# Optimization experiments

Hardware: AMD Instinct MI355X
Metric: run time of the kernel (lower is better)

Reference implementation:

```python
import jax, jax.numpy as jnp
import numpy as np

NEG_INF = -1e9


def setup_inputs() -> dict:
    key = jax.random.key(0)
    k1, k2, k3, k4 = jax.random.split(key, 4)
    B, H, M, N, D = 8, 16, 1024, 1024, 64
    return {
        "query": jax.random.normal(k1, (B, H, M, D), dtype=jnp.float32),
        "key": jax.random.normal(k2, (B, H, N, D), dtype=jnp.float32),
        "value": jax.random.normal(k3, (B, H, N, D), dtype=jnp.float32),
        "mask": jax.random.randint(k4, (B, H, N), 0, 2, dtype=jnp.int32),
    }


def reference(query, key, value, mask):
    # NOTE: faithful to source bug: scale uses key.size(-1) AFTER transpose,
    # i.e. N (sequence length), not d_h.
    N = key.shape[-2]
    scale = 1.0 / jnp.sqrt(jnp.asarray(N, dtype=query.dtype))
    # scores: [B, H, M, N]
    scores = jnp.einsum("bhmd,bhnd->bhmn", query, key) * scale
    scores = jnp.where(mask[:, :, None, :] == 0, jnp.asarray(NEG_INF, scores.dtype), scores)
    p_attn = jax.nn.softmax(scores, axis=-1)
    out = jnp.einsum("bhmn,bhnd->bhmd", p_attn, value)
    return out, p_attn
```

## Files before the change

kernel.cpp:

```cpp
#include <hip/hip_runtime.h>
#include <hip/hip_bf16.h>

#define BH 128
#define SEQ 1024
#define DH 64
#define MT 16
#define NW 256
#define PSTRIDE 1032

typedef __attribute__((ext_vector_type(8))) short short8;
typedef __attribute__((ext_vector_type(4))) float float4v;

__device__ __forceinline__ short bf16_rne(float x) {
    unsigned u = __builtin_bit_cast(unsigned, x);
    unsigned r = (u + 0x7fffu + ((u >> 16) & 1u)) >> 16;
    return (short)r;
}

__device__ __forceinline__ void bf16_split(float x, short& hi, short& lo) {
    unsigned u = __builtin_bit_cast(unsigned, x);
    hi = (short)(u >> 16);
    float hf = __builtin_bit_cast(float, u & 0xffff0000u);
    float res = x - hf;
    unsigned v = __builtin_bit_cast(unsigned, res);
    lo = (short)((v + 0x7fffu + ((v >> 16) & 1u)) >> 16);
}

__global__ __launch_bounds__(256, 2)
void Attention_66889820668421_kernel(const float* __restrict__ Q,
                                     const float* __restrict__ K,
                                     const float* __restrict__ V,
                                     const int*   __restrict__ mask,
                                     float* __restrict__ out,
                                     float* __restrict__ pattn)
{
    __shared__ short P_lds[MT * PSTRIDE];
    __shared__ float out_red[4][MT][DH];
    __shared__ float red_max[4][MT];
    __shared__ float red_sum[4][MT];

    const int tid  = threadIdx.x;
    const int wave = tid >> 6;
    const int lane = tid & 63;
    const int q    = lane >> 4;
    const int l    = lane & 15;
    const int bh   = blockIdx.y;
    const int m0   = blockIdx.x * MT;
    const int nbase = wave * NW;

    short8 a_hi[2], a_lo[2];
    {
        const float* qrow = Q + (size_t)(bh * SEQ + m0 + l) * DH;
        #pragma unroll
        for (int s = 0; s < 2; ++s) {
            float4v x0 = *(const float4v*)(qrow + s * 32 + q * 8);
            float4v x1 = *(const float4v*)(qrow + s * 32 + q * 8 + 4);
            #pragma unroll
            for (int j = 0; j < 4; ++j) {
                short h, lo2;
                bf16_split(x0[j], h, lo2); a_hi[s][j] = h; a_lo[s][j] = lo2;
                bf16_split(x1[j], h, lo2); a_hi[s][4 + j] = h; a_lo[s][4 + j] = lo2;
            }
        }
    }

    float4v acc[16];
    int mv[16];
    #pragma unroll
    for (int t = 0; t < 16; ++t) {
        const int key = nbase + t * 16 + l;
        const float* krow = K + (size_t)(bh * SEQ + key) * DH;
        float4v a = {0.f, 0.f, 0.f, 0.f};
        #pragma unroll
        for (int s = 0; s < 2; ++s) {
            float4v x0 = *(const float4v*)(krow + s * 32 + q * 8);
            float4v x1 = *(const float4v*)(krow + s * 32 + q * 8 + 4);
            short8 bhh, bll;
            #pragma unroll
            for (int j = 0; j < 4; ++j) {
                short h, lo2;
                bf16_split(x0[j], h, lo2); bhh[j] = h; bll[j] = lo2;
                bf16_split(x1[j], h, lo2); bhh[4 + j] = h; bll[4 + j] = lo2;
            }
            a = __builtin_amdgcn_mfma_f32_16x16x32_bf16(a_hi[s], bhh, a, 0, 0, 0);
            a = __builtin_amdgcn_mfma_f32_16x16x32_bf16(a_hi[s], bll, a, 0, 0, 0);
            a = __builtin_amdgcn_mfma_f32_16x16x32_bf16(a_lo[s], bhh, a, 0, 0, 0);
        }
        mv[t] = mask[bh * SEQ + nbase + t * 16 + l];
        acc[t] = a;
    }

    const float scale = 0.03125f;
    float pm[4] = {-3e38f, -3e38f, -3e38f, -3e38f};
    #pragma unroll
    for (int t = 0; t < 16; ++t) {
        const bool ok = (mv[t] != 0);
        #pragma unroll
        for (int r = 0; r < 4; ++r) {
            float s = ok ? acc[t][r] * scale : -1e9f;
            acc[t][r] = s;
            pm[r] = fmaxf(pm[r], s);
        }
    }
    #pragma unroll
    for (int off = 1; off < 16; off <<= 1) {
        #pragma unroll
        for (int r = 0; r < 4; ++r)
            pm[r] = fmaxf(pm[r], __shfl_xor(pm[r], off));
    }
    if (l == 0) {
        #pragma unroll
        for (int r = 0; r < 4; ++r) red_max[wave][q * 4 + r] = pm[r];
    }
    __syncthreads();

    float rm[4];
    #pragma unroll
    for (int r = 0; r < 4; ++r) {
        const int row = q * 4 + r;
        rm[r] = fmaxf(fmaxf(red_max[0][row], red_max[1][row]),
                      fmaxf(red_max[2][row], red_max[3][row]));
    }

    float ps[4] = {0.f, 0.f, 0.f, 0.f};
    #pragma unroll
    for (int t = 0; t < 16; ++t) {
        #pragma unroll
        for (int r = 0; r < 4; ++r) {
            float e = __expf(acc[t][r] - rm[r]);
            acc[t][r] = e;
            ps[r] += e;
        }
    }
    #pragma unroll
    for (int off = 1; off < 16; off <<= 1) {
        #pragma unroll
        for (int r = 0; r < 4; ++r)
            ps[r] += __shfl_xor(ps[r], off);
    }
    if (l == 0) {
        #pragma unroll
        for (int r = 0; r < 4; ++r) red_sum[wave][q * 4 + r] = ps[r];
    }
    __syncthreads();

    float inv[4];
    #pragma unroll
    for (int r = 0; r < 4; ++r) {
        const int row = q * 4 + r;
        inv[r] = 1.0f / (red_sum[0][row] + red_sum[1][row] +
                         red_sum[2][row] + red_sum[3][row]);
    }

    float* prow = pattn + ((size_t)bh * SEQ + m0) * SEQ;
    #pragma unroll
    for (int t = 0; t < 16; ++t) {
        const int col = nbase + t * 16 + l;
        #pragma unroll
        for (int r = 0; r < 4; ++r) {
            const int row = q * 4 + r;
            float p = acc[t][r] * inv[r];
            prow[(size_t)row * SEQ + col] = p;
            P_lds[row * PSTRIDE + col] = bf16_rne(p);
        }
    }
    __syncthreads();

    float4v ao[4];
    #pragma unroll
    for (int dt = 0; dt < 4; ++dt) ao[dt] = (float4v){0.f, 0.f, 0.f, 0.f};

    #pragma unroll 2
    for (int step = 0; step < 8; ++step) {
        const int key0 = nbase + step * 32;
        short8 pa = *(const short8*)&P_lds[l * PSTRIDE + key0 + q * 8];
        const float* vbase = V + (size_t)(bh * SEQ + key0 + q * 8) * DH + l;
        #pragma unroll
        for (int dt = 0; dt < 4; ++dt) {
            short8 vb;
            #pragma unroll
            for (int j = 0; j < 8; ++j)
                vb[j] = bf16_rne(vbase[(size_t)j * DH + dt * 16]);
            ao[dt] = __builtin_amdgcn_mfma_f32_16x16x32_bf16(pa, vb, ao[dt], 0, 0, 0);
        }
    }

    #pragma unroll
    for (int dt = 0; dt < 4; ++dt) {
        #pragma unroll
        for (int r = 0; r < 4; ++r)
            out_red[wave][q * 4 + r][dt * 16 + l] = ao[dt][r];
    }
    __syncthreads();

    #pragma unroll
    for (int i = 0; i < 4; ++i) {
        const int e = tid + 256 * i;
        const int row = e >> 6;
        const int d = e & 63;
        float s = out_red[0][row][d] + out_red[1][row][d] +
                  out_red[2][row][d] + out_red[3][row][d];
        out[(size_t)(bh * SEQ + m0 + row) * DH + d] = s;
    }
}

extern "C" void kernel_launch(void* const* d_in, const int* in_sizes, int n_in,
                              void* d_out, int out_size, void* d_ws, size_t ws_size,
                              hipStream_t stream) {
    const float* Q    = (const float*)d_in[0];
    const float* K    = (const float*)d_in[1];
    const float* V    = (const float*)d_in[2];
    const int*   mask = (const int*)d_in[3];
    float* out   = (float*)d_out;
    float* pattn = out + (size_t)BH * SEQ * DH;

    dim3 grid(SEQ / MT, BH);
    Attention_66889820668421_kernel<<<grid, 256, 0, stream>>>(Q, K, V, mask, out, pattn);
}
```

Measured before the change: 968.3 us.

## Precompute bf16 K hi/lo and transposed V in workspace before attention

Adds a prepass kernel that converts K into split bf16 hi/lo arrays and V into a bf16 layout shaped for MFMA operands, written to workspace. The main kernel then loads ready-made short8 operands instead of redoing fp32 loads and conversions in each of the 64 row-blocks per head. It also switches the P and output stores to nontemporal and raises the occupancy hint. The trade-off is an extra launch plus workspace traffic, and a fallback path remains for when the workspace is too small.

```diff
diff --git a/kernel.cpp b/kernel.cpp
--- a/kernel.cpp
+++ b/kernel.cpp
@@ -26,13 +26,228 @@
     lo = (short)((v + 0x7fffu + ((v >> 16) & 1u)) >> 16);
 }
 
-__global__ __launch_bounds__(256, 2)
+__global__ __launch_bounds__(256, 4)
+void attn_convert_kernel(const float* __restrict__ K, const float* __restrict__ V,
+                         short* __restrict__ Khi, short* __restrict__ Klo,
+                         short* __restrict__ Vt)
+{
+    const unsigned c = blockIdx.x * 256u + threadIdx.x;
+    if (blockIdx.x < 4096) {
+        const int bh = c >> 13;
+        const int o8 = c & 8191;
+        const int q  = o8 & 3;
+        const int l  = (o8 >> 2) & 15;
+        const int s  = (o8 >> 6) & 1;
+        const int kb = o8 >> 7;
+        const float* src = K + ((size_t)bh * SEQ + kb * 16 + l) * DH + s * 32 + q * 8;
+        float4v x0 = *(const float4v*)src;
+        float4v x1 = *(const float4v*)(src + 4);
+        short8 hi, lo;
+        #pragma unroll
+        for (int j = 0; j < 4; ++j) {
+            short h, w;
+            bf16_split(x0[j], h, w); hi[j] = h;     lo[j] = w;
+            bf16_split(x1[j], h, w); hi[4 + j] = h; lo[4 + j] = w;
+        }
+        *(short8*)(Khi + (size_t)c * 8) = hi;
+        *(short8*)(Klo + (size_t)c * 8) = lo;
+    } else {
+        const unsigned c2 = c - 4096u * 256u;
+        const int bh = c2 >> 13;
+        const int o8 = c2 & 8191;
+        const int lv = o8 & 15;
+        const int k8 = (o8 >> 4) & 127;
+        const int d4 = o8 >> 11;
+        const float* src = V + ((size_t)bh * SEQ + k8 * 8) * DH + d4 * 16 + lv;
+        short8 vv;
+        #pragma unroll
+        for (int j = 0; j < 8; ++j) vv[j] = bf16_rne(src[(size_t)j * DH]);
+        *(short8*)(Vt + (size_t)c2 * 8) = vv;
+    }
+}
+
+__global__ __launch_bounds__(256, 3)
 void Attention_66889820668421_kernel(const float* __restrict__ Q,
-                                     const float* __restrict__ K,
-                                     const float* __restrict__ V,
+                                     const short* __restrict__ Khi,
+                                     const short* __restrict__ Klo,
+                                     const short* __restrict__ Vt,
                                      const int*   __restrict__ mask,
                                      float* __restrict__ out,
                                      float* __restrict__ pattn)
+{
+    __shared__ short P_lds[MT * PSTRIDE];
+    __shared__ float out_red[4][MT][DH];
+    __shared__ float red_max[4][MT];
+    __shared__ float red_sum[4][MT];
+
+    const int tid  = threadIdx.x;
+    const int wave = tid >> 6;
+    const int lane = tid & 63;
+    const int q    = lane >> 4;
+    const int l    = lane & 15;
+    const int bh   = blockIdx.y;
+    const int m0   = blockIdx.x * MT;
+    const int nbase = wave * NW;
+
+    short8 a_hi[2], a_lo[2];
+    {
+        const float* qrow = Q + (size_t)(bh * SEQ + m0 + l) * DH;
+        #pragma unroll
+        for (int s = 0; s < 2; ++s) {
+            float4v x0 = *(const float4v*)(qrow + s * 32 + q * 8);
+            float4v x1 = *(const float4v*)(qrow + s * 32 + q * 8 + 4);
+            #pragma unroll
+            for (int j = 0; j < 4; ++j) {
+                short h, lo2;
+                bf16_split(x0[j], h, lo2); a_hi[s][j] = h; a_lo[s][j] = lo2;
+                bf16_split(x1[j], h, lo2); a_hi[s][4 + j] = h; a_lo[s][4 + j] = lo2;
+            }
+        }
+    }
+
+    const short* khb = Khi + ((size_t)bh << 16);
+    const short* klb = Klo + ((size_t)bh << 16);
+    const short* vtb = Vt  + ((size_t)bh << 16);
+
+    float4v acc[16];
+    int mv[16];
+    #pragma unroll
+    for (int t = 0; t < 16; ++t) {
+        const int kb   = (nbase >> 4) + t;
+        const int off0 = kb * 1024 + l * 32 + q * 8;
+        short8 b0h = *(const short8*)(khb + off0);
+        short8 b0l = *(const short8*)(klb + off0);
+        short8 b1h = *(const short8*)(khb + off0 + 512);
+        short8 b1l = *(const short8*)(klb + off0 + 512);
+        float4v a = {0.f, 0.f, 0.f, 0.f};
+        a = __builtin_amdgcn_mfma_f32_16x16x32_bf16(a_hi[0], b0h, a, 0, 0, 0);
+        a = __builtin_amdgcn_mfma_f32_16x16x32_bf16(a_hi[0], b0l, a, 0, 0, 0);
+        a = __builtin_amdgcn_mfma_f32_16x16x32_bf16(a_lo[0], b0h, a, 0, 0, 0);
+        a = __builtin_amdgcn_mfma_f32_16x16x32_bf16(a_hi[1], b1h, a, 0, 0, 0);
+        a = __builtin_amdgcn_mfma_f32_16x16x32_bf16(a_hi[1], b1l, a, 0, 0, 0);
+        a = __builtin_amdgcn_mfma_f32_16x16x32_bf16(a_lo[1], b1h, a, 0, 0, 0);
+        mv[t] = mask[bh * SEQ + nbase + t * 16 + l];
+        acc[t] = a;
+    }
+
+    const float scale = 0.03125f;
+    float pm[4] = {-3e38f, -3e38f, -3e38f, -3e38f};
+    #pragma unroll
+    for (int t = 0; t < 16; ++t) {
+        const bool ok = (mv[t] != 0);
+        #pragma unroll
+        for (int r = 0; r < 4; ++r) {
+            float s = ok ? acc[t][r] * scale : -1e9f;
+            acc[t][r] = s;
+            pm[r] = fmaxf(pm[r], s);
+        }
+    }
+    #pragma unroll
+    for (int off = 1; off < 16; off <<= 1) {
+        #pragma unroll
+        for (int r = 0; r < 4; ++r)
+            pm[r] = fmaxf(pm[r], __shfl_xor(pm[r], off));
+    }
+    if (l == 0) {
+        #pragma unroll
+        for (int r = 0; r < 4; ++r) red_max[wave][q * 4 + r] = pm[r];
+    }
+    __syncthreads();
+
+    float rm[4];
+    #pragma unroll
+    for (int r = 0; r < 4; ++r) {
+        const int row = q * 4 + r;
+        rm[r] = fmaxf(fmaxf(red_max[0][row], red_max[1][row]),
+                      fmaxf(red_max[2][row], red_max[3][row]));
+    }
+
+    float ps[4] = {0.f, 0.f, 0.f, 0.f};
+    #pragma unroll
+    for (int t = 0; t < 16; ++t) {
+        #pragma unroll
+        for (int r = 0; r < 4; ++r) {
+            float e = __expf(acc[t][r] - rm[r]);
+            acc[t][r] = e;
+            ps[r] += e;
+        }
+    }
+    #pragma unroll
+    for (int off = 1; off < 16; off <<= 1) {
+        #pragma unroll
+        for (int r = 0; r < 4; ++r)
+            ps[r] += __shfl_xor(ps[r], off);
+    }
+    if (l == 0) {
+        #pragma unroll
+        for (int r = 0; r < 4; ++r) red_sum[wave][q * 4 + r] = ps[r];
+    }
+    __syncthreads();
+
+    float inv[4];
+    #pragma unroll
+    for (int r = 0; r < 4; ++r) {
+        const int row = q * 4 + r;
+        inv[r] = 1.0f / (red_sum[0][row] + red_sum[1][row] +
+                         red_sum[2][row] + red_sum[3][row]);
+    }
+
+    float* prow = pattn + ((size_t)bh * SEQ + m0) * SEQ;
+    #pragma unroll
+    for (int t = 0; t < 16; ++t) {
+        const int col = nbase + t * 16 + l;
+        #pragma unroll
+        for (int r = 0; r < 4; ++r) {
+            const int row = q * 4 + r;
+            float p = acc[t][r] * inv[r];
+            __builtin_nontemporal_store(p, &prow[(size_t)row * SEQ + col]);
+            P_lds[row * PSTRIDE + col] = bf16_rne(p);
+        }
+    }
+    __syncthreads();
+
+    float4v ao[4];
+    #pragma unroll
+    for (int dt = 0; dt < 4; ++dt) ao[dt] = (float4v){0.f, 0.f, 0.f, 0.f};
+
+    #pragma unroll
+    for (int step = 0; step < 8; ++step) {
+        const int key0 = nbase + step * 32;
+        short8 pa = *(const short8*)&P_lds[l * PSTRIDE + key0 + q * 8];
+        const int k8q = (key0 >> 3) + q;
+        #pragma unroll
+        for (int dt = 0; dt < 4; ++dt) {
+            short8 vb = *(const short8*)(vtb + ((size_t)(dt * 128 + k8q) * 16 + l) * 8);
+            ao[dt] = __builtin_amdgcn_mfma_f32_16x16x32_bf16(pa, vb, ao[dt], 0, 0, 0);
+        }
+    }
+
+    #pragma unroll
+    for (int dt = 0; dt < 4; ++dt) {
+        #pragma unroll
+        for (int r = 0; r < 4; ++r)
+            out_red[wave][q * 4 + r][dt * 16 + l] = ao[dt][r];
+    }
+    __syncthreads();
+
+    #pragma unroll
+    for (int i = 0; i < 4; ++i) {
+        const int e = tid + 256 * i;
+        const int row = e >> 6;
+        const int d = e & 63;
+        float s = out_red[0][row][d] + out_red[1][row][d] +
+                  out_red[2][row][d] + out_red[3][row][d];
+        __builtin_nontemporal_store(s, &out[(size_t)(bh * SEQ + m0 + row) * DH + d]);
+    }
+}
+
+__global__ __launch_bounds__(256, 2)
+void Attention_66889820668421_fallback(const float* __restrict__ Q,
+                                       const float* __restrict__ K,
+                                       const float* __restrict__ V,
+                                       const int*   __restrict__ mask,
+                                       float* __restrict__ out,
+                                       float* __restrict__ pattn)
 {
     __shared__ short P_lds[MT * PSTRIDE];
     __shared__ float out_red[4][MT][DH];
@@ -214,6 +429,19 @@
     float* out   = (float*)d_out;
     float* pattn = out + (size_t)BH * SEQ * DH;
 
+    const size_t elems = (size_t)BH * SEQ * DH;
+    const size_t need  = elems * sizeof(short) * 3;
+
     dim3 grid(SEQ / MT, BH);
-    Attention_66889820668421_kernel<<<grid, 256, 0, stream>>>(Q, K, V, mask, out, pattn);
-}
+    if (ws_size >= need) {
+        short* Khi = (short*)d_ws;
+        short* Klo = Khi + elems;
+        short* Vt  = Klo + elems;
+        attn_convert_kernel<<<dim3(8192), 256, 0, stream>>>(K, V, Khi, Klo, Vt);
+        Attention_66889820668421_kernel<<<grid, 256, 0, stream>>>(Q, Khi, Klo, Vt,
+                                                                  mask, out, pattn);
+    } else {
+        Attention_66889820668421_fallback<<<grid, 256, 0, stream>>>(Q, K, V, mask,
+                                                                    out, pattn);
+    }
+}
```

Result: faster. 788.6 us (-18.6%).
